# Kernel tuning notes

Hardware: AMD Instinct MI355X
Metric: run time of the kernel (lower is better)

Reference implementation:

```python
import jax, jax.numpy as jnp
import numpy as np

N, DIN, H, OUT = 2048, 128, 64, 7


def setup_inputs() -> dict:
    key = jax.random.key(0)
    ks = jax.random.split(key, 24)

    def lin(k, out_d, in_d):
        kw, kb = jax.random.split(k)
        s = 1.0 / np.sqrt(in_d)
        W = jax.random.uniform(kw, (out_d, in_d), minval=-s, maxval=s, dtype=jnp.float32)
        b = jax.random.uniform(kb, (out_d,), minval=-s, maxval=s, dtype=jnp.float32)
        return W, b

    x = jax.random.normal(ks[0], (N, DIN), dtype=jnp.float32)
    A = jax.random.uniform(ks[1], (N, N), dtype=jnp.float32)
    W1, b1 = lin(ks[2], H, DIN)
    WF1, bF1 = lin(ks[3], H, H)
    WF2, bF2 = lin(ks[4], H, H)
    WT1, bT1 = lin(ks[5], H, H)
    WT2, bT2 = lin(ks[6], H, H)
    WC1, bC1 = lin(ks[7], H, H)
    WC2, bC2 = lin(ks[8], H, H)
    Wa, ba = lin(ks[9], H, H)
    q = jax.random.normal(ks[10], (H,), dtype=jnp.float32)
    W2, b2 = lin(ks[11], OUT, H)
    return dict(x=x, A=A, k=4, W1=W1, b1=b1, WF1=WF1, bF1=bF1, WF2=WF2, bF2=bF2,
                WT1=WT1, bT1=bT1, WT2=WT2, bT2=bT2, WC1=WC1, bC1=bC1, WC2=WC2,
                bC2=bC2, Wa=Wa, ba=ba, q=q, W2=W2, b2=b2)


def leaky(x):
    return jnp.where(x > 0, x, 0.1 * x)


def laplacian(A):
    # D^{-1/2} A D^{-1/2} with diagonal D of (rowsum + 1e-10)
    d = (jnp.sum(A, -1) + 1e-10) ** -0.5
    return A * d[:, None] * d[None, :]


def cos_sim(x):
    n = jnp.sqrt(jnp.sum(x * x, -1, keepdims=True))
    s = x / n + 1e-10  # note: +1e-10 AFTER the division, as in the source
    return s @ s.T


def heat(x):
    # exp(-0.5 * sum_d ((x_i - x_j)^2 + 1e-10)); gram trick, same math as
    # the [d, N, N] broadcasted version in the source.
    sq = jnp.sum(x * x, -1)
    dist = sq[:, None] + sq[None, :] - 2.0 * (x @ x.T) + x.shape[-1] * 1e-10
    return jnp.exp(-0.5 * dist)


def l2_norm_rows(x):
    m = jnp.sqrt(jnp.mean(x * x, -1)) + 1e-10
    return x / m[:, None]


def hsic(x1, x2):
    n = x1.shape[-2]
    K1 = x1 @ x1.T
    K2 = x2 @ x2.T
    Rm = jnp.eye(n, dtype=x1.dtype) - jnp.ones((n, n), dtype=x1.dtype) / n
    P = Rm @ K1 @ Rm  # [N, N]
    # mean(I * (P @ K2)) * n^2/(n-1)^2 = trace(P @ K2)/(n-1)^2; K2 symmetric
    return jnp.sum(P * K2) / (n - 1) ** 2


def gnn(z, Ad, W, b):
    return leaky((Ad @ z) @ W.T + b)


def reference(x, A, k, W1, b1, WF1, bF1, WF2, bF2, WT1, bT1, WT2, bT2,
              WC1, bC1, WC2, bC2, Wa, ba, q, W2, b2):
    h = leaky(x @ W1.T + b1)                       # [N, H]
    At = laplacian(A)
    Hh = heat(h)                                    # [N, N]
    rank = jnp.argsort(jnp.argsort(-Hh, axis=-1), axis=-1)  # double-argsort rank
    mask = (rank < k).astype(h.dtype)
    Af = laplacian(cos_sim(h) * mask)
    zf = gnn(gnn(h, Af, WF1, bF1), Af, WF2, bF2)
    zt = gnn(gnn(h, At, WT1, bT1), At, WT2, bT2)
    zcf = gnn(gnn(h, Af, WC1, bC1), Af, WC2, bC2)
    zct = gnn(gnn(h, At, WC1, bC1), At, WC2, bC2)
    Lcf = l2_norm_rows(zcf)
    Lct = l2_norm_rows(zct)
    Lc = jnp.mean((Lcf @ Lcf.T - Lct @ Lct.T) ** 2)
    Ld = hsic(zt, zct) + hsic(zf, zcf)
    zc = (zcf + zct) / 2
    z = jnp.stack([zf, zt, zc], axis=-2)            # [N, 3, H]
    a = jax.nn.softmax(jnp.tanh(z @ Wa.T + ba) @ q, axis=-1)  # [N, 3]
    zagg = jnp.einsum('nkd,nk->nd', z, a)           # [N, H]
    out = zagg @ W2.T + b2                          # [N, OUT]
    return (out, Lc, Ld)
```

## Files before the change

### kernel.cpp

```cpp
#include <hip/hip_runtime.h>
#include <stdint.h>

#define N 2048
#define DIN 128
#define H 64
#define OUTD 7
#define RS 32
#define S1 8
#define S2 8

#define Z_ZT  0
#define Z_ZCT 64
#define Z_ZF  128
#define Z_ZCF 192
#define Z_LCF 256
#define Z_LCT 320

typedef short bf16x8 __attribute__((ext_vector_type(8)));
typedef float floatx4 __attribute__((ext_vector_type(4)));

__device__ __forceinline__ float leaky(float x){ return x > 0.f ? x : 0.1f*x; }

__device__ __forceinline__ unsigned short f2bf(float f){
  unsigned int u = __float_as_uint(f);
  u = u + 0x7FFFu + ((u >> 16) & 1u);
  return (unsigned short)(u >> 16);
}

__device__ __forceinline__ float waveRedSum(float v){
  #pragma unroll
  for (int o = 32; o > 0; o >>= 1) v += __shfl_xor(v, o, 64);
  return v;
}

__device__ __forceinline__ unsigned long long shflx64(unsigned long long v, int m){
  unsigned int lo = (unsigned int)v, hi = (unsigned int)(v >> 32);
  lo = (unsigned int)__shfl_xor((int)lo, m, 64);
  hi = (unsigned int)__shfl_xor((int)hi, m, 64);
  return ((unsigned long long)hi << 32) | lo;
}

__global__ void k_prep(const float* __restrict__ A, float* __restrict__ dA,
                       unsigned short* __restrict__ Abf){
  int i = blockIdx.x;
  const float4* row = (const float4*)(A + (size_t)i * N);
  unsigned short* ob = Abf + (size_t)i * N;
  float s = 0.f;
  #pragma unroll
  for (int it = 0; it < 2; it++){
    int u = threadIdx.x + it*256;
    float4 v = row[u];
    s += v.x + v.y + v.z + v.w;
    ushort4 o;
    o.x = f2bf(v.x); o.y = f2bf(v.y); o.z = f2bf(v.z); o.w = f2bf(v.w);
    *(ushort4*)&ob[u*4] = o;
  }
  __shared__ float red[4];
  s = waveRedSum(s);
  int wid = threadIdx.x >> 6, lane = threadIdx.x & 63;
  if (lane == 0) red[wid] = s;
  __syncthreads();
  if (threadIdx.x == 0){
    float t = red[0] + red[1] + red[2] + red[3];
    dA[i] = 1.0f / sqrtf(t + 1e-10f);
  }
}

__global__ __launch_bounds__(256) void k_h(const float* __restrict__ x,
                    const float* __restrict__ W1g, const float* __restrict__ b1,
                    const float* __restrict__ dA,
                    float* __restrict__ h, unsigned short* __restrict__ hsT,
                    float* __restrict__ sq, float* __restrict__ hsum){
  __shared__ float W1t[DIN][H+1];
  __shared__ float xb[4][DIN];
  __shared__ __align__(16) unsigned short hTb[H][16];
  int tid = threadIdx.x, w = tid >> 6, t = tid & 63;
  int i0 = blockIdx.x * 16;
  for (int u = tid; u < 2048; u += 256){
    float4 g = ((const float4*)W1g)[u];
    int row = u >> 5, c0 = (u & 31) * 4;
    W1t[c0+0][row] = g.x; W1t[c0+1][row] = g.y;
    W1t[c0+2][row] = g.z; W1t[c0+3][row] = g.w;
  }
  __syncthreads();
  float bt = b1[t];
  for (int rr = 0; rr < 4; rr++){
    int i = i0 + w*4 + rr;
    xb[w][t]      = x[(size_t)i*DIN + t];
    xb[w][t + 64] = x[(size_t)i*DIN + t + 64];
    float acc = bt;
    #pragma unroll
    for (int c4 = 0; c4 < DIN/4; c4++){
      float xv[4]; *(float4*)xv = *(const float4*)&xb[w][c4*4];
      acc += xv[0]*W1t[c4*4+0][t] + xv[1]*W1t[c4*4+1][t]
           + xv[2]*W1t[c4*4+2][t] + xv[3]*W1t[c4*4+3][t];
    }
    float hv = leaky(acc);
    h[(size_t)i*H + t] = hv;
    hTb[t][w*4+rr] = f2bf(dA[i]*hv);
    float s2 = waveRedSum(hv*hv);
    float s1 = waveRedSum(hv);
    if (t == 0){ sq[i] = s2; hsum[i] = s1; }
  }
  __syncthreads();
  { int c = tid >> 2, qq = tid & 3;
    ushort4 v = *(ushort4*)&hTb[c][qq*4];
    *(ushort4*)&hsT[(size_t)c*N + i0 + qq*4] = v; }
}

__global__ __launch_bounds__(256) void k_gram(const float* __restrict__ h,
                                              float* __restrict__ DOT){
  __shared__ float at[32][132];
  __shared__ float bt[32][132];
  int bi = blockIdx.x, bj = blockIdx.y;
  int tid = threadIdx.x;
  int rg = tid >> 4, cg = tid & 15;
  float acc[8][8] = {};
  for (int kc = 0; kc < 64; kc += 32){
    for (int u = tid; u < 1024; u += 256){
      int row = u >> 3, k4 = u & 7;
      float4 v = *(const float4*)(h + (size_t)(bi*128 + row)*H + kc + k4*4);
      at[k4*4+0][row] = v.x; at[k4*4+1][row] = v.y;
      at[k4*4+2][row] = v.z; at[k4*4+3][row] = v.w;
    }
    for (int u = tid; u < 1024; u += 256){
      int row = u >> 3, k4 = u & 7;
      float4 v = *(const float4*)(h + (size_t)(bj*128 + row)*H + kc + k4*4);
      bt[k4*4+0][row] = v.x; bt[k4*4+1][row] = v.y;
      bt[k4*4+2][row] = v.z; bt[k4*4+3][row] = v.w;
    }
    __syncthreads();
    for (int k = 0; k < 32; k++){
      float a[8], b[8];
      *(float4*)&a[0] = *(const float4*)&at[k][rg*8];
      *(float4*)&a[4] = *(const float4*)&at[k][rg*8+4];
      *(float4*)&b[0] = *(const float4*)&bt[k][cg*8];
      *(float4*)&b[4] = *(const float4*)&bt[k][cg*8+4];
      #pragma unroll
      for (int ii = 0; ii < 8; ii++)
        #pragma unroll
        for (int jj = 0; jj < 8; jj++)
          acc[ii][jj] += a[ii]*b[jj];
    }
    __syncthreads();
  }
  #pragma unroll
  for (int ii = 0; ii < 8; ii++){
    int r = bi*128 + rg*8 + ii;
    float* out = DOT + (size_t)r*N + bj*128 + cg*8;
    *(float4*)(out)   = make_float4(acc[ii][0], acc[ii][1], acc[ii][2], acc[ii][3]);
    *(float4*)(out+4) = make_float4(acc[ii][4], acc[ii][5], acc[ii][6], acc[ii][7]);
  }
}

__global__ __launch_bounds__(256) void k_topk(const float* __restrict__ DOT,
      const float* __restrict__ sq, const float* __restrict__ hsum,
      int* __restrict__ nidx, float* __restrict__ ncos, float* __restrict__ df){
  int i = blockIdx.x, tid = threadIdx.x;
  __shared__ unsigned long long cand[1024];
  const float4* row = (const float4*)(DOT + (size_t)i * N);
  const float4* sq4 = (const float4*)sq;
  unsigned long long best[4] = {~0ULL, ~0ULL, ~0ULL, ~0ULL};
  #pragma unroll
  for (int blk = 0; blk < 2; blk++){
    int u = tid + blk*256;
    float4 d = row[u];
    float4 s = sq4[u];
    float kv[4] = { s.x - 2.f*d.x, s.y - 2.f*d.y, s.z - 2.f*d.z, s.w - 2.f*d.w };
    #pragma unroll
    for (int e = 0; e < 4; e++){
      unsigned int j = (unsigned int)(u*4 + e);
      unsigned int uk = __float_as_uint(kv[e]);
      uk = (uk & 0x80000000u) ? ~uk : (uk | 0x80000000u);
      unsigned long long c = ((unsigned long long)uk << 32) | j;
      if (c < best[3]){
        best[3] = c;
        unsigned long long t0;
        if (best[3] < best[2]){ t0 = best[2]; best[2] = best[3]; best[3] = t0; }
        if (best[2] < best[1]){ t0 = best[1]; best[1] = best[2]; best[2] = t0; }
        if (best[1] < best[0]){ t0 = best[0]; best[0] = best[1]; best[1] = t0; }
      }
    }
  }
  #pragma unroll
  for (int e = 0; e < 4; e++) cand[e*256 + tid] = best[e];
  __syncthreads();
  if (tid < 64){
    unsigned long long loc[16];
    #pragma unroll
    for (int e = 0; e < 16; e++) loc[e] = cand[e*64 + tid];
    unsigned long long w0=~0ULL, w1=~0ULL, w2=~0ULL, w3=~0ULL;
    #pragma unroll
    for (int r = 0; r < 4; r++){
      unsigned long long m = loc[0];
      #pragma unroll
      for (int e = 1; e < 16; e++) m = (loc[e] < m) ? loc[e] : m;
      unsigned long long g = m;
      #pragma unroll
      for (int o = 32; o > 0; o >>= 1){
        unsigned long long other = shflx64(g, o);
        if (other < g) g = other;
      }
      #pragma unroll
      for (int e = 0; e < 16; e++) if (loc[e] == g) loc[e] = ~0ULL;
      if (r == 0) w0 = g; else if (r == 1) w1 = g; else if (r == 2) w2 = g; else w3 = g;
    }
    float myc = 0.f;
    if (tid < 4){
      unsigned long long w = (tid==0) ? w0 : (tid==1) ? w1 : (tid==2) ? w2 : w3;
      unsigned int j = (unsigned int)w;
      unsigned int uk = (unsigned int)(w >> 32);
      float key = (uk & 0x80000000u) ? __uint_as_float(uk ^ 0x80000000u)
                                     : __uint_as_float(~uk);
      float sqj = sq[j];
      float dot = (sqj - key) * 0.5f;
      float hni = sqrtf(sq[i]), hnj = sqrtf(sqj);
      float cosv = dot/(hni*hnj)
                 + 1e-10f*(hsum[i]/hni + hsum[j]/hnj)
                 + 64.0f*1e-20f;
      nidx[i*4 + tid] = (int)j;
      ncos[i*4 + tid] = cosv;
      myc = cosv;
    }
    myc += __shfl_xor(myc, 1, 64);
    myc += __shfl_xor(myc, 2, 64);
    if (tid == 0) df[i] = 1.f / sqrtf(myc + 1e-10f);
  }
}

template<int BN>
__global__ __launch_bounds__(256) void k_mgemm(
    const unsigned short* __restrict__ Abf, const unsigned short* __restrict__ BtG,
    float* __restrict__ Cp, int KC){
  __shared__ __align__(16) unsigned short Asl[64][72];
  __shared__ __align__(16) unsigned short Bsl[BN][72];
  int m0 = blockIdx.x * 64, kbase = blockIdx.y * KC;
  int tid = threadIdx.x;
  int w = tid >> 6, lane = tid & 63;
  int quad = lane >> 4, ml = lane & 15;
  floatx4 acc[BN/16];
  #pragma unroll
  for (int ct = 0; ct < BN/16; ct++) acc[ct] = (floatx4){0.f,0.f,0.f,0.f};

  for (int kc = 0; kc < KC; kc += 64){
    int kb = kbase + kc;
    #pragma unroll
    for (int u = tid; u < 512; u += 256){
      int r = u >> 3, s = u & 7;
      *(uint4*)&Asl[r][s*8] = *(const uint4*)(Abf + ((size_t)(m0+r) << 11) + kb + s*8);
    }
    #pragma unroll
    for (int u = tid; u < BN*8; u += 256){
      int n = u >> 3, s = u & 7;
      *(uint4*)&Bsl[n][s*8] = *(const uint4*)(BtG + ((size_t)n << 11) + kb + s*8);
    }
    __syncthreads();
    #pragma unroll
    for (int k0 = 0; k0 < 64; k0 += 32){
      bf16x8 af = *(const bf16x8*)&Asl[16*w + ml][k0 + quad*8];
      #pragma unroll
      for (int ct = 0; ct < BN/16; ct++){
        bf16x8 bfr = *(const bf16x8*)&Bsl[16*ct + ml][k0 + quad*8];
        acc[ct] = __builtin_amdgcn_mfma_f32_16x16x32_bf16(af, bfr, acc[ct], 0, 0, 0);
      }
    }
    __syncthreads();
  }
  float* C = Cp + (size_t)blockIdx.y * (N * BN);
  #pragma unroll
  for (int ct = 0; ct < BN/16; ct++)
    #pragma unroll
    for (int r = 0; r < 4; r++){
      int row = m0 + 16*w + quad*4 + r;
      C[(size_t)row*BN + 16*ct + ml] = acc[ct][r];
    }
}

__global__ __launch_bounds__(256) void k_sumY1(const float* __restrict__ Y1p,
    const float* __restrict__ dA, float* __restrict__ Y1s){
  int idx4 = blockIdx.x*256 + threadIdx.x;
  int i = idx4 >> 4;
  float4 s = ((const float4*)Y1p)[idx4];
  #pragma unroll
  for (int p = 1; p < S1; p++){
    float4 v = ((const float4*)Y1p)[(size_t)p*(N*H/4) + idx4];
    s.x += v.x; s.y += v.y; s.z += v.z; s.w += v.w;
  }
  float d = dA[i];
  s.x *= d; s.y *= d; s.z *= d; s.w *= d;
  ((float4*)Y1s)[idx4] = s;
}

__global__ __launch_bounds__(256) void k_sumY2(const float* __restrict__ Y2p,
    const float* __restrict__ dA, float* __restrict__ Y2s){
  int idx4 = blockIdx.x*256 + threadIdx.x;
  int i = idx4 >> 5;
  float4 s = ((const float4*)Y2p)[idx4];
  #pragma unroll
  for (int p = 1; p < S2; p++){
    float4 v = ((const float4*)Y2p)[(size_t)p*(N*128/4) + idx4];
    s.x += v.x; s.y += v.y; s.z += v.z; s.w += v.w;
  }
  float d = dA[i];
  s.x *= d; s.y *= d; s.z *= d; s.w *= d;
  ((float4*)Y2s)[idx4] = s;
}

__global__ __launch_bounds__(256) void k_z1(const float* __restrict__ h,
                     const int* __restrict__ nidx, const float* __restrict__ ncos,
                     const float* __restrict__ df, const float* __restrict__ Y1s,
                     const float* __restrict__ dA,
                     const float* __restrict__ WF1g, const float* __restrict__ bF1,
                     const float* __restrict__ WC1g, const float* __restrict__ bC1,
                     const float* __restrict__ WT1g, const float* __restrict__ bT1,
                     float* __restrict__ z1f, float* __restrict__ z1cf,
                     unsigned short* __restrict__ ZsT){
  __shared__ float Wf[H][H+1], Wc[H][H+1], Wt[H][H+1];
  __shared__ float vb[4][H], ub[4][H];
  __shared__ __align__(16) unsigned short Zb[128][16];
  int tid = threadIdx.x, w = tid >> 6, t = tid & 63;
  int i0 = blockIdx.x * 16;
  for (int u = tid; u < 1024; u += 256){
    int row = u >> 4, c0 = (u & 15) * 4;
    float4 f = ((const float4*)WF1g)[u];
    Wf[c0+0][row]=f.x; Wf[c0+1][row]=f.y; Wf[c0+2][row]=f.z; Wf[c0+3][row]=f.w;
    float4 g = ((const float4*)WC1g)[u];
    Wc[c0+0][row]=g.x; Wc[c0+1][row]=g.y; Wc[c0+2][row]=g.z; Wc[c0+3][row]=g.w;
    float4 e = ((const float4*)WT1g)[u];
    Wt[c0+0][row]=e.x; Wt[c0+1][row]=e.y; Wt[c0+2][row]=e.z; Wt[c0+3][row]=e.w;
  }
  __syncthreads();
  float bfv = bF1[t], bcv = bC1[t], btv = bT1[t];
  for (int rr = 0; rr < 4; rr++){
    int i = i0 + w*4 + rr;
    int j0 = nidx[i*4], j1 = nidx[i*4+1], j2 = nidx[i*4+2], j3 = nidx[i*4+3];
    float di = df[i];
    float w0 = ncos[i*4]  *di*df[j0];
    float w1 = ncos[i*4+1]*di*df[j1];
    float w2 = ncos[i*4+2]*di*df[j2];
    float w3 = ncos[i*4+3]*di*df[j3];
    vb[w][t] = w0*h[(size_t)j0*H+t] + w1*h[(size_t)j1*H+t]
             + w2*h[(size_t)j2*H+t] + w3*h[(size_t)j3*H+t];
    ub[w][t] = Y1s[(size_t)i*H + t];
    float a1 = bfv, a2 = bcv, a3 = btv, a4 = bcv;
    #pragma unroll
    for (int c4 = 0; c4 < 16; c4++){
      float vv[4], uv[4];
      *(float4*)vv = *(const float4*)&vb[w][c4*4];
      *(float4*)uv = *(const float4*)&ub[w][c4*4];
      #pragma unroll
      for (int e = 0; e < 4; e++){
        int c = c4*4 + e;
        float wfv = Wf[c][t], wcv = Wc[c][t], wtv = Wt[c][t];
        a1 += vv[e]*wfv; a2 += vv[e]*wcv;
        a3 += uv[e]*wtv; a4 += uv[e]*wcv;
      }
    }
    z1f [(size_t)i*H+t] = leaky(a1);
    z1cf[(size_t)i*H+t] = leaky(a2);
    float dai = dA[i];
    int lr = w*4 + rr;
    Zb[t][lr]      = f2bf(dai*leaky(a3));
    Zb[64+t][lr]   = f2bf(dai*leaky(a4));
  }
  __syncthreads();
  { int c = tid >> 1, hh = tid & 1;
    uint4 v = *(uint4*)&Zb[c][hh*8];
    *(uint4*)&ZsT[(size_t)c*N + i0 + hh*8] = v; }
}

__global__ __launch_bounds__(256) void k_z2o(const float* __restrict__ z1f,
                      const float* __restrict__ z1cf,
                      const int* __restrict__ nidx, const float* __restrict__ ncos,
                      const float* __restrict__ df, const float* __restrict__ Y2s,
                      const float* __restrict__ WF2g, const float* __restrict__ bF2,
                      const float* __restrict__ WC2g, const float* __restrict__ bC2,
                      const float* __restrict__ WT2g, const float* __restrict__ bT2,
                      const float* __restrict__ Wag, const float* __restrict__ ba,
                      const float* __restrict__ q,  const float* __restrict__ W2,
                      const float* __restrict__ b2,
                      float* __restrict__ Z6, float* __restrict__ out){
  __shared__ float Wf[H][H+1], Wc[H][H+1], Wt2[H][H+1], Wal[H][H+1];
  __shared__ float vf[4][H], vc[4][H], ut[4][H], uc[4][H];
  __shared__ float zfb[4][H], ztb[4][H], zcb[4][H], zab[4][H];
  int tid = threadIdx.x, w = tid >> 6, t = tid & 63;
  int i0 = blockIdx.x * 16;
  for (int u = tid; u < 1024; u += 256){
    int row = u >> 4, c0 = (u & 15) * 4;
    float4 f = ((const float4*)WF2g)[u];
    Wf[c0+0][row]=f.x; Wf[c0+1][row]=f.y; Wf[c0+2][row]=f.z; Wf[c0+3][row]=f.w;
    float4 g = ((const float4*)WC2g)[u];
    Wc[c0+0][row]=g.x; Wc[c0+1][row]=g.y; Wc[c0+2][row]=g.z; Wc[c0+3][row]=g.w;
    float4 e = ((const float4*)WT2g)[u];
    Wt2[c0+0][row]=e.x; Wt2[c0+1][row]=e.y; Wt2[c0+2][row]=e.z; Wt2[c0+3][row]=e.w;
    float4 a = ((const float4*)Wag)[u];
    Wal[c0+0][row]=a.x; Wal[c0+1][row]=a.y; Wal[c0+2][row]=a.z; Wal[c0+3][row]=a.w;
  }
  __syncthreads();
  float bfv = bF2[t], bcv = bC2[t], btv = bT2[t];
  float bav = ba[t], qv = q[t];
  for (int rr = 0; rr < 4; rr++){
    int i = i0 + w*4 + rr;
    int j0 = nidx[i*4], j1 = nidx[i*4+1], j2 = nidx[i*4+2], j3 = nidx[i*4+3];
    float di = df[i];
    float w0 = ncos[i*4]  *di*df[j0];
    float w1 = ncos[i*4+1]*di*df[j1];
    float w2 = ncos[i*4+2]*di*df[j2];
    float w3 = ncos[i*4+3]*di*df[j3];
    vf[w][t] = w0*z1f[(size_t)j0*H+t] + w1*z1f[(size_t)j1*H+t]
             + w2*z1f[(size_t)j2*H+t] + w3*z1f[(size_t)j3*H+t];
    vc[w][t] = w0*z1cf[(size_t)j0*H+t] + w1*z1cf[(size_t)j1*H+t]
             + w2*z1cf[(size_t)j2*H+t] + w3*z1cf[(size_t)j3*H+t];
    ut[w][t] = Y2s[(size_t)i*128 + t];
    uc[w][t] = Y2s[(size_t)i*128 + 64 + t];
    float a1 = bfv, a2 = bcv, a3 = btv, a4 = bcv;
    #pragma unroll
    for (int c4 = 0; c4 < 16; c4++){
      float fv[4], cv[4], tv[4], uv[4];
      *(float4*)fv = *(const float4*)&vf[w][c4*4];
      *(float4*)cv = *(const float4*)&vc[w][c4*4];
      *(float4*)tv = *(const float4*)&ut[w][c4*4];
      *(float4*)uv = *(const float4*)&uc[w][c4*4];
      #pragma unroll
      for (int e = 0; e < 4; e++){
        int c = c4*4 + e;
        float wfv = Wf[c][t], wcv = Wc[c][t], wtv = Wt2[c][t];
        a1 += fv[e]*wfv; a2 += cv[e]*wcv;
        a3 += tv[e]*wtv; a4 += uv[e]*wcv;
      }
    }
    float zfv = leaky(a1), zcfv = leaky(a2), ztv = leaky(a3), zctv = leaky(a4);
    float* zr = Z6 + (size_t)i*384;
    zr[Z_ZF + t] = zfv;  zr[Z_ZT + t] = ztv;
    zr[Z_ZCF + t] = zcfv; zr[Z_ZCT + t] = zctv;
    float scf = waveRedSum(zcfv*zcfv);
    float mcf = sqrtf(scf*(1.f/64.f)) + 1e-10f;
    zr[Z_LCF + t] = zcfv/mcf;
    float sct = waveRedSum(zctv*zctv);
    float mct = sqrtf(sct*(1.f/64.f)) + 1e-10f;
    zr[Z_LCT + t] = zctv/mct;
    float zcv = 0.5f*(zcfv + zctv);
    zfb[w][t] = zfv; ztb[w][t] = ztv; zcb[w][t] = zcv;
    float ev[3];
    #pragma unroll
    for (int kk = 0; kk < 3; kk++){
      const float* zsrc = (kk == 0) ? zfb[w] : (kk == 1) ? ztb[w] : zcb[w];
      float aa = bav;
      #pragma unroll
      for (int c4 = 0; c4 < 16; c4++){
        float zv[4]; *(float4*)zv = *(const float4*)&zsrc[c4*4];
        #pragma unroll
        for (int e = 0; e < 4; e++) aa += zv[e]*Wal[c4*4+e][t];
      }
      ev[kk] = waveRedSum(tanhf(aa)*qv);
    }
    float mx = fmaxf(ev[0], fmaxf(ev[1], ev[2]));
    float x0 = expf(ev[0]-mx), x1 = expf(ev[1]-mx), x2 = expf(ev[2]-mx);
    float inv = 1.f/(x0+x1+x2);
    float zagg = x0*inv*zfv + x1*inv*ztv + x2*inv*zcv;
    zab[w][t] = zagg;
    if (t < OUTD){
      float acc2 = b2[t];
      const float4* w2r = (const float4*)(W2 + (size_t)t*H);
      #pragma unroll
      for (int c4 = 0; c4 < 16; c4++){
        float4 wv = w2r[c4];
        float zv[4]; *(float4*)zv = *(const float4*)&zab[w][c4*4];
        acc2 += zv[0]*wv.x + zv[1]*wv.y + zv[2]*wv.z + zv[3]*wv.w;
      }
      out[(size_t)i*OUTD + t] = acc2;
    }
  }
}

__global__ __launch_bounds__(256) void k_reduce(const float* __restrict__ Z6,
                                                float* __restrict__ redP,
                                                float* __restrict__ colP){
  __shared__ float sa[64][68];
  __shared__ float sb[64][68];
  int p = blockIdx.x >> 5;
  int s = blockIdx.x & 31;
  int tid = threadIdx.x;
  const int aoffT[5] = {Z_ZT,  Z_ZF,  Z_LCF, Z_LCF, Z_LCT};
  const int boffT[5] = {Z_ZCT, Z_ZCF, Z_LCF, Z_LCT, Z_LCT};
  int aoff = aoffT[p], boff = boffT[p];
  int r0 = s * 64;
  {
    int row = tid >> 4, c4 = (tid & 15) * 4;
    #pragma unroll
    for (int rr = 0; rr < 64; rr += 16){
      const float* zr = Z6 + (size_t)(r0 + row + rr) * 384;
      *(float4*)&sa[row + rr][c4] = *(const float4*)&zr[aoff + c4];
      *(float4*)&sb[row + rr][c4] = *(const float4*)&zr[boff + c4];
    }
  }
  __syncthreads();
  int rg = tid >> 4, cg = tid & 15;
  float acc[4][4] = {};
  #pragma unroll 8
  for (int k = 0; k < 64; k++){
    float a[4], b[4];
    *(float4*)a = *(const float4*)&sa[k][rg*4];
    *(float4*)b = *(const float4*)&sb[k][cg*4];
    #pragma unroll
    for (int ii = 0; ii < 4; ii++)
      #pragma unroll
      for (int jj = 0; jj < 4; jj++)
        acc[ii][jj] += a[ii]*b[jj];
  }
  float* rp = redP + (size_t)blockIdx.x * 4096;
  #pragma unroll
  for (int ii = 0; ii < 4; ii++)
    *(float4*)&rp[(rg*4+ii)*64 + cg*4] =
      make_float4(acc[ii][0], acc[ii][1], acc[ii][2], acc[ii][3]);
  if (p < 2 && tid < 128){
    int t = tid & 63;
    float csum = 0.f;
    if (tid < 64){
      #pragma unroll 16
      for (int r = 0; r < 64; r++) csum += sa[r][t];
    } else {
      #pragma unroll 16
      for (int r = 0; r < 64; r++) csum += sb[r][t];
    }
    colP[((size_t)p*RS + s)*128 + tid] = csum;
  }
}

__global__ void k_combine(const float* __restrict__ redP,
                          const float* __restrict__ colP,
                          float* __restrict__ red){
  int idx = blockIdx.x*256 + threadIdx.x;
  if (idx < 20480){
    int p = idx >> 12, i = idx & 4095;
    float sum = 0.f;
    #pragma unroll 8
    for (int s = 0; s < RS; s++) sum += redP[((size_t)p*RS + s)*4096 + i];
    red[idx] = sum;
  } else if (idx < 20736){
    int j = idx - 20480;
    int p = j >> 7, rem = j & 127;
    float sum = 0.f;
    #pragma unroll 8
    for (int s = 0; s < RS; s++) sum += colP[((size_t)p*RS + s)*128 + rem];
    red[idx] = sum;
  }
}

__global__ void k_final(const float* __restrict__ red, float* __restrict__ out2){
  int tid = threadIdx.x;
  const float* Stc = red;
  const float* Sfc = red + 4096;
  const float* Cff = red + 8192;
  const float* Cft = red + 12288;
  const float* Ctt = red + 16384;
  const float* cst = red + 20480;
  const float* csct= red + 20544;
  const float* csf = red + 20608;
  const float* cscf= red + 20672;
  float sCff=0, sCft=0, sCtt=0, sM1=0, sM2=0;
  for (int u = tid*16; u < tid*16+16; u++){
    int d = u >> 6, e = u & 63;
    float m1 = Stc[u] - cst[d]*csct[e]*(1.f/2048.f);
    float m2 = Sfc[u] - csf[d]*cscf[e]*(1.f/2048.f);
    sM1 += m1*m1; sM2 += m2*m2;
    float cf = Cff[u], cx = Cft[u], ct = Ctt[u];
    sCff += cf*cf; sCft += cx*cx; sCtt += ct*ct;
  }
  __shared__ float rd[5][4];
  sCff = waveRedSum(sCff); sCft = waveRedSum(sCft); sCtt = waveRedSum(sCtt);
  sM1 = waveRedSum(sM1);   sM2 = waveRedSum(sM2);
  int w = tid >> 6, lane = tid & 63;
  if (lane == 0){ rd[0][w]=sCff; rd[1][w]=sCft; rd[2][w]=sCtt; rd[3][w]=sM1; rd[4][w]=sM2; }
  __syncthreads();
  if (tid == 0){
    float A0 = rd[0][0]+rd[0][1]+rd[0][2]+rd[0][3];
    float A1 = rd[1][0]+rd[1][1]+rd[1][2]+rd[1][3];
    float A2 = rd[2][0]+rd[2][1]+rd[2][2]+rd[2][3];
    float M1 = rd[3][0]+rd[3][1]+rd[3][2]+rd[3][3];
    float M2 = rd[4][0]+rd[4][1]+rd[4][2]+rd[4][3];
    out2[0] = (A0 - 2.f*A1 + A2) * (1.f/(2048.f*2048.f));
    out2[1] = (M1 + M2) * (1.f/(2047.f*2047.f));
  }
}

extern "C" void kernel_launch(void* const* d_in, const int* in_sizes, int n_in,
                              void* d_out, int out_size, void* d_ws, size_t ws_size,
                              hipStream_t stream) {
  const float* x   = (const float*)d_in[0];
  const float* A   = (const float*)d_in[1];
  const float* W1  = (const float*)d_in[3];
  const float* b1  = (const float*)d_in[4];
  const float* WF1 = (const float*)d_in[5];
  const float* bF1 = (const float*)d_in[6];
  const float* WF2 = (const float*)d_in[7];
  const float* bF2 = (const float*)d_in[8];
  const float* WT1 = (const float*)d_in[9];
  const float* bT1 = (const float*)d_in[10];
  const float* WT2 = (const float*)d_in[11];
  const float* bT2 = (const float*)d_in[12];
  const float* WC1 = (const float*)d_in[13];
  const float* bC1 = (const float*)d_in[14];
  const float* WC2 = (const float*)d_in[15];
  const float* bC2 = (const float*)d_in[16];
  const float* Wa  = (const float*)d_in[17];
  const float* ba  = (const float*)d_in[18];
  const float* q   = (const float*)d_in[19];
  const float* W2  = (const float*)d_in[20];
  const float* b2  = (const float*)d_in[21];
  float* out = (float*)d_out;

  float* W = (float*)d_ws;
  float* h_   = W;
  float* dA   = h_  + N*H;
  float* sq   = dA  + N;
  float* hsum = sq  + N;
  float* df   = hsum+ N;
  int*   nidx = (int*)(df + N);
  float* ncos = (float*)(nidx + N*4);
  float* red  = ncos + N*4;
  float* DOT  = red + 20736;
  float* Z6   = DOT + (size_t)N*N;
  float* Y1p  = Z6  + (size_t)N*384;
  float* Y2p  = Y1p + (size_t)S1*N*H;
  float* Y1s  = Y2p + (size_t)S2*N*128;
  float* Y2s  = Y1s + (size_t)N*H;
  float* z1f  = Y2s + (size_t)N*128;
  float* z1cf = z1f + N*H;
  float* redP = z1cf+ N*H;
  float* colP = redP+ 655360;
  unsigned short* Abf = (unsigned short*)(colP + 8192);
  unsigned short* hsT = Abf + (size_t)N*N;
  unsigned short* ZsT = hsT + (size_t)H*N;

  k_prep<<<N, 256, 0, stream>>>(A, dA, Abf);
  k_h<<<128, 256, 0, stream>>>(x, W1, b1, dA, h_, hsT, sq, hsum);
  k_gram<<<dim3(16,16), 256, 0, stream>>>(h_, DOT);
  k_topk<<<N, 256, 0, stream>>>(DOT, sq, hsum, nidx, ncos, df);

  k_mgemm<64><<<dim3(32,S1), 256, 0, stream>>>(Abf, hsT, Y1p, N/S1);
  k_sumY1<<<128, 256, 0, stream>>>(Y1p, dA, Y1s);
  k_z1<<<128, 256, 0, stream>>>(h_, nidx, ncos, df, Y1s, dA,
                                WF1, bF1, WC1, bC1, WT1, bT1, z1f, z1cf, ZsT);
  k_mgemm<128><<<dim3(32,S2), 256, 0, stream>>>(Abf, ZsT, Y2p, N/S2);
  k_sumY2<<<256, 256, 0, stream>>>(Y2p, dA, Y2s);
  k_z2o<<<128, 256, 0, stream>>>(z1f, z1cf, nidx, ncos, df, Y2s,
                                 WF2, bF2, WC2, bC2, WT2, bT2,
                                 Wa, ba, q, W2, b2, Z6, out);
  k_reduce<<<5*RS, 256, 0, stream>>>(Z6, redP, colP);
  k_combine<<<81, 256, 0, stream>>>(redP, colP, red);
  k_final<<<1, 256, 0, stream>>>(red, out + (size_t)N*OUTD);
}
```

Baseline: 232.6 us.

## Split GNN layer kernels into gather, bf16 MFMA dense, and attention kernels

The fused per-row scalar-FMA kernels k_z1 and k_z2o are replaced by three stages: separate sparse-gather kernels, MFMA bf16 64x64 GEMM kernels parallelised over four weight/input pairs, and a separate attention/output kernel. The sums of the partial A@X products are now stored as bf16 to feed the MFMA operands directly. The aim is to remove the low-parallelism scalar matmul work (only 128 blocks before) and put the dense parts on matrix cores. The cost is extra launches, extra global round trips for the intermediates, and lower precision for the layer inputs and weights.

```diff
diff --git a/kernel.cpp b/kernel.cpp
--- a/kernel.cpp
+++ b/kernel.cpp
@@ -277,7 +277,7 @@
 }
 
 __global__ __launch_bounds__(256) void k_sumY1(const float* __restrict__ Y1p,
-    const float* __restrict__ dA, float* __restrict__ Y1s){
+    const float* __restrict__ dA, unsigned short* __restrict__ Ub1){
   int idx4 = blockIdx.x*256 + threadIdx.x;
   int i = idx4 >> 4;
   float4 s = ((const float4*)Y1p)[idx4];
@@ -287,12 +287,13 @@
     s.x += v.x; s.y += v.y; s.z += v.z; s.w += v.w;
   }
   float d = dA[i];
-  s.x *= d; s.y *= d; s.z *= d; s.w *= d;
-  ((float4*)Y1s)[idx4] = s;
+  ushort4 o;
+  o.x = f2bf(s.x*d); o.y = f2bf(s.y*d); o.z = f2bf(s.z*d); o.w = f2bf(s.w*d);
+  ((ushort4*)Ub1)[idx4] = o;
 }
 
 __global__ __launch_bounds__(256) void k_sumY2(const float* __restrict__ Y2p,
-    const float* __restrict__ dA, float* __restrict__ Y2s){
+    const float* __restrict__ dA, unsigned short* __restrict__ Ub2){
   int idx4 = blockIdx.x*256 + threadIdx.x;
   int i = idx4 >> 5;
   float4 s = ((const float4*)Y2p)[idx4];
@@ -302,174 +303,233 @@
     s.x += v.x; s.y += v.y; s.z += v.z; s.w += v.w;
   }
   float d = dA[i];
-  s.x *= d; s.y *= d; s.z *= d; s.w *= d;
-  ((float4*)Y2s)[idx4] = s;
-}
-
-__global__ __launch_bounds__(256) void k_z1(const float* __restrict__ h,
-                     const int* __restrict__ nidx, const float* __restrict__ ncos,
-                     const float* __restrict__ df, const float* __restrict__ Y1s,
-                     const float* __restrict__ dA,
-                     const float* __restrict__ WF1g, const float* __restrict__ bF1,
-                     const float* __restrict__ WC1g, const float* __restrict__ bC1,
-                     const float* __restrict__ WT1g, const float* __restrict__ bT1,
-                     float* __restrict__ z1f, float* __restrict__ z1cf,
-                     unsigned short* __restrict__ ZsT){
-  __shared__ float Wf[H][H+1], Wc[H][H+1], Wt[H][H+1];
-  __shared__ float vb[4][H], ub[4][H];
-  __shared__ __align__(16) unsigned short Zb[128][16];
+  ushort4 o;
+  o.x = f2bf(s.x*d); o.y = f2bf(s.y*d); o.z = f2bf(s.z*d); o.w = f2bf(s.w*d);
+  ((ushort4*)Ub2)[idx4] = o;
+}
+
+__global__ __launch_bounds__(256) void k_gather1(const float* __restrict__ h,
+    const int* __restrict__ nidx, const float* __restrict__ ncos,
+    const float* __restrict__ df, unsigned short* __restrict__ Vb1){
   int tid = threadIdx.x, w = tid >> 6, t = tid & 63;
-  int i0 = blockIdx.x * 16;
+  int i = blockIdx.x*4 + w;
+  int j0 = nidx[i*4], j1 = nidx[i*4+1], j2 = nidx[i*4+2], j3 = nidx[i*4+3];
+  float di = df[i];
+  float w0 = ncos[i*4]  *di*df[j0];
+  float w1 = ncos[i*4+1]*di*df[j1];
+  float w2 = ncos[i*4+2]*di*df[j2];
+  float w3 = ncos[i*4+3]*di*df[j3];
+  float v = w0*h[(size_t)j0*H+t] + w1*h[(size_t)j1*H+t]
+          + w2*h[(size_t)j2*H+t] + w3*h[(size_t)j3*H+t];
+  Vb1[(size_t)i*H + t] = f2bf(v);
+}
+
+__global__ __launch_bounds__(256) void k_gather2(const float* __restrict__ z1f,
+    const float* __restrict__ z1cf,
+    const int* __restrict__ nidx, const float* __restrict__ ncos,
+    const float* __restrict__ df,
+    unsigned short* __restrict__ Vf2, unsigned short* __restrict__ Vc2){
+  int tid = threadIdx.x, w = tid >> 6, t = tid & 63;
+  int i = blockIdx.x*4 + w;
+  int j0 = nidx[i*4], j1 = nidx[i*4+1], j2 = nidx[i*4+2], j3 = nidx[i*4+3];
+  float di = df[i];
+  float w0 = ncos[i*4]  *di*df[j0];
+  float w1 = ncos[i*4+1]*di*df[j1];
+  float w2 = ncos[i*4+2]*di*df[j2];
+  float w3 = ncos[i*4+3]*di*df[j3];
+  float vf = w0*z1f[(size_t)j0*H+t] + w1*z1f[(size_t)j1*H+t]
+           + w2*z1f[(size_t)j2*H+t] + w3*z1f[(size_t)j3*H+t];
+  float vc = w0*z1cf[(size_t)j0*H+t] + w1*z1cf[(size_t)j1*H+t]
+           + w2*z1cf[(size_t)j2*H+t] + w3*z1cf[(size_t)j3*H+t];
+  Vf2[(size_t)i*H + t] = f2bf(vf);
+  Vc2[(size_t)i*H + t] = f2bf(vc);
+}
+
+__global__ __launch_bounds__(256) void k_z1m(
+    const unsigned short* __restrict__ Vb1, const unsigned short* __restrict__ Ub1,
+    const float* __restrict__ WF1, const float* __restrict__ WC1,
+    const float* __restrict__ WT1, const float* __restrict__ bF1,
+    const float* __restrict__ bC1, const float* __restrict__ bT1,
+    const float* __restrict__ dA,
+    float* __restrict__ z1f, float* __restrict__ z1cf,
+    unsigned short* __restrict__ ZsT){
+  __shared__ __align__(16) unsigned short Vs[64][72];
+  __shared__ __align__(16) unsigned short Ws[64][72];
+  __shared__ __align__(16) unsigned short Tb[64][72];
+  __shared__ float bias[64], dAl[64];
+  int p = blockIdx.y, i0 = blockIdx.x * 64, tid = threadIdx.x;
+  const unsigned short* Vsrc = (p < 2) ? Vb1 : Ub1;
+  const float* Wsrc = (p == 0) ? WF1 : (p == 2) ? WT1 : WC1;
+  const float* bsrc = (p == 0) ? bF1 : (p == 2) ? bT1 : bC1;
+  #pragma unroll
+  for (int u = tid; u < 512; u += 256){
+    int r = u >> 3, s = u & 7;
+    *(uint4*)&Vs[r][s*8] = *(const uint4*)(Vsrc + (size_t)(i0+r)*H + s*8);
+  }
   for (int u = tid; u < 1024; u += 256){
-    int row = u >> 4, c0 = (u & 15) * 4;
-    float4 f = ((const float4*)WF1g)[u];
-    Wf[c0+0][row]=f.x; Wf[c0+1][row]=f.y; Wf[c0+2][row]=f.z; Wf[c0+3][row]=f.w;
-    float4 g = ((const float4*)WC1g)[u];
-    Wc[c0+0][row]=g.x; Wc[c0+1][row]=g.y; Wc[c0+2][row]=g.z; Wc[c0+3][row]=g.w;
-    float4 e = ((const float4*)WT1g)[u];
-    Wt[c0+0][row]=e.x; Wt[c0+1][row]=e.y; Wt[c0+2][row]=e.z; Wt[c0+3][row]=e.w;
-  }
-  __syncthreads();
-  float bfv = bF1[t], bcv = bC1[t], btv = bT1[t];
-  for (int rr = 0; rr < 4; rr++){
-    int i = i0 + w*4 + rr;
-    int j0 = nidx[i*4], j1 = nidx[i*4+1], j2 = nidx[i*4+2], j3 = nidx[i*4+3];
-    float di = df[i];
-    float w0 = ncos[i*4]  *di*df[j0];
-    float w1 = ncos[i*4+1]*di*df[j1];
-    float w2 = ncos[i*4+2]*di*df[j2];
-    float w3 = ncos[i*4+3]*di*df[j3];
-    vb[w][t] = w0*h[(size_t)j0*H+t] + w1*h[(size_t)j1*H+t]
-             + w2*h[(size_t)j2*H+t] + w3*h[(size_t)j3*H+t];
-    ub[w][t] = Y1s[(size_t)i*H + t];
-    float a1 = bfv, a2 = bcv, a3 = btv, a4 = bcv;
-    #pragma unroll
-    for (int c4 = 0; c4 < 16; c4++){
-      float vv[4], uv[4];
-      *(float4*)vv = *(const float4*)&vb[w][c4*4];
-      *(float4*)uv = *(const float4*)&ub[w][c4*4];
-      #pragma unroll
-      for (int e = 0; e < 4; e++){
-        int c = c4*4 + e;
-        float wfv = Wf[c][t], wcv = Wc[c][t], wtv = Wt[c][t];
-        a1 += vv[e]*wfv; a2 += vv[e]*wcv;
-        a3 += uv[e]*wtv; a4 += uv[e]*wcv;
+    int r = u >> 4, c4 = (u & 15)*4;
+    float4 f = *(const float4*)(Wsrc + (size_t)r*H + c4);
+    Ws[r][c4+0] = f2bf(f.x); Ws[r][c4+1] = f2bf(f.y);
+    Ws[r][c4+2] = f2bf(f.z); Ws[r][c4+3] = f2bf(f.w);
+  }
+  if (tid < 64){ bias[tid] = bsrc[tid]; dAl[tid] = dA[i0 + tid]; }
+  __syncthreads();
+  int w = tid >> 6, lane = tid & 63, quad = lane >> 4, ml = lane & 15;
+  floatx4 acc[4];
+  #pragma unroll
+  for (int ct = 0; ct < 4; ct++) acc[ct] = (floatx4){0.f,0.f,0.f,0.f};
+  #pragma unroll
+  for (int k0 = 0; k0 < 64; k0 += 32){
+    bf16x8 af = *(const bf16x8*)&Vs[16*w + ml][k0 + quad*8];
+    #pragma unroll
+    for (int ct = 0; ct < 4; ct++){
+      bf16x8 bfr = *(const bf16x8*)&Ws[16*ct + ml][k0 + quad*8];
+      acc[ct] = __builtin_amdgcn_mfma_f32_16x16x32_bf16(af, bfr, acc[ct], 0, 0, 0);
+    }
+  }
+  if (p < 2){
+    float* dst = (p == 0) ? z1f : z1cf;
+    #pragma unroll
+    for (int ct = 0; ct < 4; ct++){
+      int col = 16*ct + ml;
+      #pragma unroll
+      for (int r = 0; r < 4; r++){
+        int row = 16*w + quad*4 + r;
+        dst[(size_t)(i0+row)*H + col] = leaky(acc[ct][r] + bias[col]);
       }
     }
-    z1f [(size_t)i*H+t] = leaky(a1);
-    z1cf[(size_t)i*H+t] = leaky(a2);
-    float dai = dA[i];
-    int lr = w*4 + rr;
-    Zb[t][lr]      = f2bf(dai*leaky(a3));
-    Zb[64+t][lr]   = f2bf(dai*leaky(a4));
-  }
-  __syncthreads();
-  { int c = tid >> 1, hh = tid & 1;
-    uint4 v = *(uint4*)&Zb[c][hh*8];
-    *(uint4*)&ZsT[(size_t)c*N + i0 + hh*8] = v; }
-}
-
-__global__ __launch_bounds__(256) void k_z2o(const float* __restrict__ z1f,
-                      const float* __restrict__ z1cf,
-                      const int* __restrict__ nidx, const float* __restrict__ ncos,
-                      const float* __restrict__ df, const float* __restrict__ Y2s,
-                      const float* __restrict__ WF2g, const float* __restrict__ bF2,
-                      const float* __restrict__ WC2g, const float* __restrict__ bC2,
-                      const float* __restrict__ WT2g, const float* __restrict__ bT2,
-                      const float* __restrict__ Wag, const float* __restrict__ ba,
-                      const float* __restrict__ q,  const float* __restrict__ W2,
-                      const float* __restrict__ b2,
-                      float* __restrict__ Z6, float* __restrict__ out){
-  __shared__ float Wf[H][H+1], Wc[H][H+1], Wt2[H][H+1], Wal[H][H+1];
-  __shared__ float vf[4][H], vc[4][H], ut[4][H], uc[4][H];
-  __shared__ float zfb[4][H], ztb[4][H], zcb[4][H], zab[4][H];
+  } else {
+    #pragma unroll
+    for (int ct = 0; ct < 4; ct++){
+      int col = 16*ct + ml;
+      #pragma unroll
+      for (int r = 0; r < 4; r++){
+        int row = 16*w + quad*4 + r;
+        Tb[col][row] = f2bf(dAl[row] * leaky(acc[ct][r] + bias[col]));
+      }
+    }
+    __syncthreads();
+    int zb = (p == 2) ? 0 : 64;
+    #pragma unroll
+    for (int u = tid; u < 512; u += 256){
+      int c = u >> 3, s = u & 7;
+      *(uint4*)&ZsT[(size_t)(zb + c)*N + i0 + s*8] = *(uint4*)&Tb[c][s*8];
+    }
+  }
+}
+
+__global__ __launch_bounds__(256) void k_z2m(
+    const unsigned short* __restrict__ Vf2, const unsigned short* __restrict__ Vc2,
+    const unsigned short* __restrict__ Ub2,
+    const float* __restrict__ WF2, const float* __restrict__ WC2,
+    const float* __restrict__ WT2, const float* __restrict__ bF2,
+    const float* __restrict__ bC2, const float* __restrict__ bT2,
+    float* __restrict__ Z6){
+  __shared__ __align__(16) unsigned short Vs[64][72];
+  __shared__ __align__(16) unsigned short Ws[64][72];
+  __shared__ float bias[64];
+  int p = blockIdx.y, i0 = blockIdx.x * 64, tid = threadIdx.x;
+  const unsigned short* vptr = (p == 0) ? Vf2 : (p == 1) ? Vc2 : Ub2;
+  int vstride = (p < 2) ? 64 : 128;
+  int voff = (p == 3) ? 64 : 0;
+  const float* Wsrc = (p == 0) ? WF2 : (p == 2) ? WT2 : WC2;
+  const float* bsrc = (p == 0) ? bF2 : (p == 2) ? bT2 : bC2;
+  #pragma unroll
+  for (int u = tid; u < 512; u += 256){
+    int r = u >> 3, s = u & 7;
+    *(uint4*)&Vs[r][s*8] = *(const uint4*)(vptr + (size_t)(i0+r)*vstride + voff + s*8);
+  }
+  for (int u = tid; u < 1024; u += 256){
+    int r = u >> 4, c4 = (u & 15)*4;
+    float4 f = *(const float4*)(Wsrc + (size_t)r*H + c4);
+    Ws[r][c4+0] = f2bf(f.x); Ws[r][c4+1] = f2bf(f.y);
+    Ws[r][c4+2] = f2bf(f.z); Ws[r][c4+3] = f2bf(f.w);
+  }
+  if (tid < 64) bias[tid] = bsrc[tid];
+  __syncthreads();
+  int w = tid >> 6, lane = tid & 63, quad = lane >> 4, ml = lane & 15;
+  floatx4 acc[4];
+  #pragma unroll
+  for (int ct = 0; ct < 4; ct++) acc[ct] = (floatx4){0.f,0.f,0.f,0.f};
+  #pragma unroll
+  for (int k0 = 0; k0 < 64; k0 += 32){
+    bf16x8 af = *(const bf16x8*)&Vs[16*w + ml][k0 + quad*8];
+    #pragma unroll
+    for (int ct = 0; ct < 4; ct++){
+      bf16x8 bfr = *(const bf16x8*)&Ws[16*ct + ml][k0 + quad*8];
+      acc[ct] = __builtin_amdgcn_mfma_f32_16x16x32_bf16(af, bfr, acc[ct], 0, 0, 0);
+    }
+  }
+  int zoff = (p == 0) ? Z_ZF : (p == 1) ? Z_ZCF : (p == 2) ? Z_ZT : Z_ZCT;
+  float val[4][4];
+  #pragma unroll
+  for (int ct = 0; ct < 4; ct++){
+    int col = 16*ct + ml;
+    #pragma unroll
+    for (int r = 0; r < 4; r++){
+      val[ct][r] = leaky(acc[ct][r] + bias[col]);
+      int row = 16*w + quad*4 + r;
+      Z6[(size_t)(i0+row)*384 + zoff + col] = val[ct][r];
+    }
+  }
+  if (p == 1 || p == 3){
+    int loff = (p == 1) ? Z_LCF : Z_LCT;
+    #pragma unroll
+    for (int r = 0; r < 4; r++){
+      float s = val[0][r]*val[0][r] + val[1][r]*val[1][r]
+              + val[2][r]*val[2][r] + val[3][r]*val[3][r];
+      s += __shfl_xor(s, 1, 64); s += __shfl_xor(s, 2, 64);
+      s += __shfl_xor(s, 4, 64); s += __shfl_xor(s, 8, 64);
+      float m = sqrtf(s*(1.f/64.f)) + 1e-10f;
+      int row = 16*w + quad*4 + r;
+      #pragma unroll
+      for (int ct = 0; ct < 4; ct++)
+        Z6[(size_t)(i0+row)*384 + loff + 16*ct + ml] = val[ct][r]/m;
+    }
+  }
+}
+
+__global__ __launch_bounds__(256) void k_att(const float* __restrict__ Z6,
+    const float* __restrict__ Wag, const float* __restrict__ ba,
+    const float* __restrict__ q, const float* __restrict__ W2g,
+    const float* __restrict__ b2, float* __restrict__ out){
+  __shared__ float Wal[64][65];
+  __shared__ float W2l[448];
+  __shared__ float zbuf[4][3][66];
+  __shared__ float zagg[4][66];
   int tid = threadIdx.x, w = tid >> 6, t = tid & 63;
-  int i0 = blockIdx.x * 16;
   for (int u = tid; u < 1024; u += 256){
-    int row = u >> 4, c0 = (u & 15) * 4;
-    float4 f = ((const float4*)WF2g)[u];
-    Wf[c0+0][row]=f.x; Wf[c0+1][row]=f.y; Wf[c0+2][row]=f.z; Wf[c0+3][row]=f.w;
-    float4 g = ((const float4*)WC2g)[u];
-    Wc[c0+0][row]=g.x; Wc[c0+1][row]=g.y; Wc[c0+2][row]=g.z; Wc[c0+3][row]=g.w;
-    float4 e = ((const float4*)WT2g)[u];
-    Wt2[c0+0][row]=e.x; Wt2[c0+1][row]=e.y; Wt2[c0+2][row]=e.z; Wt2[c0+3][row]=e.w;
-    float4 a = ((const float4*)Wag)[u];
-    Wal[c0+0][row]=a.x; Wal[c0+1][row]=a.y; Wal[c0+2][row]=a.z; Wal[c0+3][row]=a.w;
-  }
-  __syncthreads();
-  float bfv = bF2[t], bcv = bC2[t], btv = bT2[t];
+    int r = u >> 4, c4 = (u & 15)*4;
+    float4 f = ((const float4*)Wag)[u];
+    Wal[r][c4+0]=f.x; Wal[r][c4+1]=f.y; Wal[r][c4+2]=f.z; Wal[r][c4+3]=f.w;
+  }
+  if (tid < 112) *(float4*)&W2l[tid*4] = ((const float4*)W2g)[tid];
+  __syncthreads();
+  int i = blockIdx.x*4 + w;
+  const float* zr = Z6 + (size_t)i*384;
+  float zf = zr[Z_ZF + t], zt = zr[Z_ZT + t];
+  float zc = 0.5f*(zr[Z_ZCF + t] + zr[Z_ZCT + t]);
+  zbuf[w][0][t] = zf; zbuf[w][1][t] = zt; zbuf[w][2][t] = zc;
+  __syncthreads();
   float bav = ba[t], qv = q[t];
-  for (int rr = 0; rr < 4; rr++){
-    int i = i0 + w*4 + rr;
-    int j0 = nidx[i*4], j1 = nidx[i*4+1], j2 = nidx[i*4+2], j3 = nidx[i*4+3];
-    float di = df[i];
-    float w0 = ncos[i*4]  *di*df[j0];
-    float w1 = ncos[i*4+1]*di*df[j1];
-    float w2 = ncos[i*4+2]*di*df[j2];
-    float w3 = ncos[i*4+3]*di*df[j3];
-    vf[w][t] = w0*z1f[(size_t)j0*H+t] + w1*z1f[(size_t)j1*H+t]
-             + w2*z1f[(size_t)j2*H+t] + w3*z1f[(size_t)j3*H+t];
-    vc[w][t] = w0*z1cf[(size_t)j0*H+t] + w1*z1cf[(size_t)j1*H+t]
-             + w2*z1cf[(size_t)j2*H+t] + w3*z1cf[(size_t)j3*H+t];
-    ut[w][t] = Y2s[(size_t)i*128 + t];
-    uc[w][t] = Y2s[(size_t)i*128 + 64 + t];
-    float a1 = bfv, a2 = bcv, a3 = btv, a4 = bcv;
-    #pragma unroll
-    for (int c4 = 0; c4 < 16; c4++){
-      float fv[4], cv[4], tv[4], uv[4];
-      *(float4*)fv = *(const float4*)&vf[w][c4*4];
-      *(float4*)cv = *(const float4*)&vc[w][c4*4];
-      *(float4*)tv = *(const float4*)&ut[w][c4*4];
-      *(float4*)uv = *(const float4*)&uc[w][c4*4];
-      #pragma unroll
-      for (int e = 0; e < 4; e++){
-        int c = c4*4 + e;
-        float wfv = Wf[c][t], wcv = Wc[c][t], wtv = Wt2[c][t];
-        a1 += fv[e]*wfv; a2 += cv[e]*wcv;
-        a3 += tv[e]*wtv; a4 += uv[e]*wcv;
-      }
-    }
-    float zfv = leaky(a1), zcfv = leaky(a2), ztv = leaky(a3), zctv = leaky(a4);
-    float* zr = Z6 + (size_t)i*384;
-    zr[Z_ZF + t] = zfv;  zr[Z_ZT + t] = ztv;
-    zr[Z_ZCF + t] = zcfv; zr[Z_ZCT + t] = zctv;
-    float scf = waveRedSum(zcfv*zcfv);
-    float mcf = sqrtf(scf*(1.f/64.f)) + 1e-10f;
-    zr[Z_LCF + t] = zcfv/mcf;
-    float sct = waveRedSum(zctv*zctv);
-    float mct = sqrtf(sct*(1.f/64.f)) + 1e-10f;
-    zr[Z_LCT + t] = zctv/mct;
-    float zcv = 0.5f*(zcfv + zctv);
-    zfb[w][t] = zfv; ztb[w][t] = ztv; zcb[w][t] = zcv;
-    float ev[3];
-    #pragma unroll
-    for (int kk = 0; kk < 3; kk++){
-      const float* zsrc = (kk == 0) ? zfb[w] : (kk == 1) ? ztb[w] : zcb[w];
-      float aa = bav;
-      #pragma unroll
-      for (int c4 = 0; c4 < 16; c4++){
-        float zv[4]; *(float4*)zv = *(const float4*)&zsrc[c4*4];
-        #pragma unroll
-        for (int e = 0; e < 4; e++) aa += zv[e]*Wal[c4*4+e][t];
-      }
-      ev[kk] = waveRedSum(tanhf(aa)*qv);
-    }
-    float mx = fmaxf(ev[0], fmaxf(ev[1], ev[2]));
-    float x0 = expf(ev[0]-mx), x1 = expf(ev[1]-mx), x2 = expf(ev[2]-mx);
-    float inv = 1.f/(x0+x1+x2);
-    float zagg = x0*inv*zfv + x1*inv*ztv + x2*inv*zcv;
-    zab[w][t] = zagg;
-    if (t < OUTD){
-      float acc2 = b2[t];
-      const float4* w2r = (const float4*)(W2 + (size_t)t*H);
-      #pragma unroll
-      for (int c4 = 0; c4 < 16; c4++){
-        float4 wv = w2r[c4];
-        float zv[4]; *(float4*)zv = *(const float4*)&zab[w][c4*4];
-        acc2 += zv[0]*wv.x + zv[1]*wv.y + zv[2]*wv.z + zv[3]*wv.w;
-      }
-      out[(size_t)i*OUTD + t] = acc2;
-    }
+  float e[3];
+  #pragma unroll
+  for (int k = 0; k < 3; k++){
+    float S = bav;
+    #pragma unroll 8
+    for (int c = 0; c < 64; c++) S += zbuf[w][k][c] * Wal[t][c];
+    e[k] = waveRedSum(tanhf(S)*qv);
+  }
+  float mx = fmaxf(e[0], fmaxf(e[1], e[2]));
+  float x0 = expf(e[0]-mx), x1 = expf(e[1]-mx), x2 = expf(e[2]-mx);
+  float inv = 1.f/(x0+x1+x2);
+  zagg[w][t] = x0*inv*zf + x1*inv*zt + x2*inv*zc;
+  __syncthreads();
+  if (t < OUTD){
+    float acc = b2[t];
+    #pragma unroll 8
+    for (int c = 0; c < 64; c++) acc += zagg[w][c]*W2l[t*64 + c];
+    out[(size_t)i*OUTD + t] = acc;
   }
 }
 
@@ -623,30 +683,35 @@
   float* Z6   = DOT + (size_t)N*N;
   float* Y1p  = Z6  + (size_t)N*384;
   float* Y2p  = Y1p + (size_t)S1*N*H;
-  float* Y1s  = Y2p + (size_t)S2*N*128;
-  float* Y2s  = Y1s + (size_t)N*H;
-  float* z1f  = Y2s + (size_t)N*128;
+  float* z1f  = Y2p + (size_t)S2*N*128;
   float* z1cf = z1f + N*H;
   float* redP = z1cf+ N*H;
   float* colP = redP+ 655360;
   unsigned short* Abf = (unsigned short*)(colP + 8192);
   unsigned short* hsT = Abf + (size_t)N*N;
   unsigned short* ZsT = hsT + (size_t)H*N;
+  unsigned short* Vb1 = ZsT + (size_t)128*N;
+  unsigned short* Ub1 = Vb1 + (size_t)N*H;
+  unsigned short* Vf2 = Ub1 + (size_t)N*H;
+  unsigned short* Vc2 = Vf2 + (size_t)N*H;
+  unsigned short* Ub2 = Vc2 + (size_t)N*H;
 
   k_prep<<<N, 256, 0, stream>>>(A, dA, Abf);
   k_h<<<128, 256, 0, stream>>>(x, W1, b1, dA, h_, hsT, sq, hsum);
   k_gram<<<dim3(16,16), 256, 0, stream>>>(h_, DOT);
   k_topk<<<N, 256, 0, stream>>>(DOT, sq, hsum, nidx, ncos, df);
+  k_gather1<<<512, 256, 0, stream>>>(h_, nidx, ncos, df, Vb1);
 
   k_mgemm<64><<<dim3(32,S1), 256, 0, stream>>>(Abf, hsT, Y1p, N/S1);
-  k_sumY1<<<128, 256, 0, stream>>>(Y1p, dA, Y1s);
-  k_z1<<<128, 256, 0, stream>>>(h_, nidx, ncos, df, Y1s, dA,
-                                WF1, bF1, WC1, bC1, WT1, bT1, z1f, z1cf, ZsT);
+  k_sumY1<<<128, 256, 0, stream>>>(Y1p, dA, Ub1);
+  k_z1m<<<dim3(32,4), 256, 0, stream>>>(Vb1, Ub1, WF1, WC1, WT1, bF1, bC1, bT1,
+                                        dA, z1f, z1cf, ZsT);
   k_mgemm<128><<<dim3(32,S2), 256, 0, stream>>>(Abf, ZsT, Y2p, N/S2);
-  k_sumY2<<<256, 256, 0, stream>>>(Y2p, dA, Y2s);
-  k_z2o<<<128, 256, 0, stream>>>(z1f, z1cf, nidx, ncos, df, Y2s,
-                                 WF2, bF2, WC2, bC2, WT2, bT2,
-                                 Wa, ba, q, W2, b2, Z6, out);
+  k_sumY2<<<256, 256, 0, stream>>>(Y2p, dA, Ub2);
+  k_gather2<<<512, 256, 0, stream>>>(z1f, z1cf, nidx, ncos, df, Vf2, Vc2);
+  k_z2m<<<dim3(32,4), 256, 0, stream>>>(Vf2, Vc2, Ub2, WF2, WC2, WT2,
+                                        bF2, bC2, bT2, Z6);
+  k_att<<<512, 256, 0, stream>>>(Z6, Wa, ba, q, W2, b2, out);
   k_reduce<<<5*RS, 256, 0, stream>>>(Z6, redP, colP);
   k_combine<<<81, 256, 0, stream>>>(redP, colP, red);
   k_final<<<1, 256, 0, stream>>>(red, out + (size_t)N*OUTD);
```

Measured after the change: 204.1 us. 12.3% less time.
